# Kernel tuning notes

Hardware: AMD Instinct MI355X
Metric: run time of the kernel (lower is better)

Reference implementation:

```python
import jax, jax.numpy as jnp
import numpy as np

D_MODEL = 1024
NUM_HEADS = 16
DEPTH = D_MODEL // NUM_HEADS
MAX_LEN = 5000
B, S = 4, 1024


def _dense(x, W, b):
    return x @ W + b


def _split_heads(x, n_heads, depth):
    # [..., S, D] -> [..., H, S, depth]
    *lead, s, d = x.shape
    x = x.reshape(*lead, s, n_heads, depth)
    return jnp.swapaxes(x, -3, -2)


def setup_inputs() -> dict:
    key = jax.random.key(0)
    ks = jax.random.split(key, 12)
    w = 0.02  # glorot-ish scale to keep softmax logits sane
    inp = {
        'q': jax.random.normal(ks[0], (B, S, D_MODEL), jnp.float32),
        'k': jax.random.normal(ks[1], (B, S, D_MODEL), jnp.float32),
        'v': jax.random.normal(ks[2], (B, S, D_MODEL), jnp.float32),
        'Wq': jax.random.normal(ks[3], (D_MODEL, D_MODEL), jnp.float32) * w,
        'bq': jnp.zeros((D_MODEL,), jnp.float32),
        'Wk': jax.random.normal(ks[4], (D_MODEL, D_MODEL), jnp.float32) * w,
        'bk': jnp.zeros((D_MODEL,), jnp.float32),
        'Wv': jax.random.normal(ks[5], (D_MODEL, D_MODEL), jnp.float32) * w,
        'bv': jnp.zeros((D_MODEL,), jnp.float32),
        'Uq': jax.random.normal(ks[6], (D_MODEL, D_MODEL), jnp.float32) * w,
        'buq': jnp.zeros((D_MODEL,), jnp.float32),
        'Uk': jax.random.normal(ks[7], (D_MODEL, D_MODEL), jnp.float32) * w,
        'buk': jnp.zeros((D_MODEL,), jnp.float32),
        'pos_table': jax.random.normal(ks[8], (MAX_LEN, D_MODEL), jnp.float32) * w,
        'theta_cc': jnp.zeros((1, NUM_HEADS, 1, 1), jnp.float32),
        'theta_co': jnp.zeros((1, NUM_HEADS, 1, 1), jnp.float32),
        'theta_oc': jnp.zeros((1, NUM_HEADS, 1, 1), jnp.float32),
        'Wo': jax.random.normal(ks[9], (D_MODEL, D_MODEL), jnp.float32) * w,
        'bo': jnp.zeros((D_MODEL,), jnp.float32),
    }
    return inp


def reference(q, k, v, Wq, bq, Wk, bk, Wv, bv, Uq, buq, Uk, buk,
              pos_table, theta_cc, theta_co, theta_oc, Wo, bo):
    b, s, d = q.shape
    # content projections -> [B,H,S,depth]
    q_c = _split_heads(_dense(q, Wq, bq), NUM_HEADS, DEPTH)
    k_c = _split_heads(_dense(k, Wk, bk), NUM_HEADS, DEPTH)
    v_c = _split_heads(_dense(v, Wv, bv), NUM_HEADS, DEPTH)
    content_scores = jnp.einsum('bhqd,bhkd->bhqk', q_c, k_c)

    # untied positional scores (shared across batch): [1,H,S,S]
    pos_emb = pos_table[:s]                               # [S,D]
    q_p = _split_heads(_dense(pos_emb, Uq, buq)[None], NUM_HEADS, DEPTH)
    k_p = _split_heads(_dense(pos_emb, Uk, buk)[None], NUM_HEADS, DEPTH)
    pos_scores = jnp.einsum('bhqd,bhkd->bhqk', q_p, k_p)  # [1,H,S,S]

    # CLS-row/col overrides with learnable thetas
    pos_scores = pos_scores.at[:, :, 1:, 0:1].set(jnp.broadcast_to(theta_oc, (1, NUM_HEADS, s - 1, 1)))
    pos_scores = pos_scores.at[:, :, 0:1, 1:].set(jnp.broadcast_to(theta_co, (1, NUM_HEADS, 1, s - 1)))
    pos_scores = pos_scores.at[:, :, 0:1, 0:1].set(theta_cc)

    scores = (content_scores + pos_scores) / jnp.sqrt(jnp.float32(DEPTH))
    attn = jax.nn.softmax(scores, axis=-1)
    out = jnp.einsum('bhqk,bhkd->bhqd', attn, v_c)        # [B,H,S,depth]
    out = jnp.swapaxes(out, 1, 2).reshape(b, s, d)        # [B,S,D]
    return _dense(out, Wo, bo)
```

## Files before the change

kernel.cpp:

```cpp
#include <hip/hip_runtime.h>
#include <hip/hip_bf16.h>

typedef __hip_bfloat16 bf16;
typedef unsigned short u16;
typedef __attribute__((ext_vector_type(8))) short short8;
typedef __attribute__((ext_vector_type(4))) float f32x4;

#define D_MODEL 1024
#define NUM_HEADS 16
#define DEPTH 64
#define BATCH 4
#define SEQ 1024
#define BS (BATCH * SEQ)

__device__ __forceinline__ float ldDyn(const void* p, size_t i, int isbf) {
  return isbf ? __bfloat162float(((const bf16*)p)[i]) : ((const float*)p)[i];
}
__device__ __forceinline__ u16 f2bf(float f) {
  bf16 h = __float2bfloat16(f);
  return *(u16*)&h;
}
__device__ __forceinline__ void gl2lds16(const void* g, void* l) {
  __builtin_amdgcn_global_load_lds((const __attribute__((address_space(1))) unsigned int*)g,
                                   (__attribute__((address_space(3))) unsigned int*)l, 16, 0, 0);
}

__global__ void detect_kernel(const u16* __restrict__ q, int* __restrict__ flag) {
  if (threadIdx.x == 0 && blockIdx.x == 0) {
    int sane = 0;
    for (int i = 0; i < 64; ++i) {
      u16 h = q[2 * i];
      int e = (h >> 7) & 0xFF;
      if (e >= 100 && e <= 150) ++sane;
    }
    *flag = (sane >= 48) ? 1 : 0;
  }
}

__global__ __launch_bounds__(256) void convert_in(
    const void* __restrict__ q, const void* __restrict__ k, const void* __restrict__ v,
    const void* __restrict__ pos, u16* __restrict__ Qb, u16* __restrict__ Kb,
    u16* __restrict__ Vb, u16* __restrict__ Pb, const int* __restrict__ flagp) {
  const int isbf = *flagp;
  const int z = blockIdx.z;
  const void* src = (z == 0) ? q : (z == 1) ? k : (z == 2) ? v : pos;
  u16* dst = (z == 0) ? Qb : (z == 1) ? Kb : (z == 2) ? Vb : Pb;
  const size_t n8 = ((z == 3) ? (size_t)SEQ * D_MODEL : (size_t)BS * D_MODEL) / 8;
  for (size_t i = (size_t)blockIdx.x * 256 + threadIdx.x; i < n8; i += (size_t)gridDim.x * 256) {
    short8 o;
    if (isbf) {
      o = ((const short8*)src)[i];
    } else {
      const float4* f = (const float4*)src + 2 * i;
      float4 lo = f[0], hi = f[1];
      u16* pv = (u16*)&o;
      pv[0] = f2bf(lo.x); pv[1] = f2bf(lo.y); pv[2] = f2bf(lo.z); pv[3] = f2bf(lo.w);
      pv[4] = f2bf(hi.x); pv[5] = f2bf(hi.y); pv[6] = f2bf(hi.z); pv[7] = f2bf(hi.w);
    }
    ((short8*)dst)[i] = o;
  }
}

__global__ __launch_bounds__(256) void transpose_w(
    const void* W0, const void* W1, const void* W2, const void* W3, const void* W4,
    const void* W5, u16* __restrict__ WT, const int* __restrict__ flagp) {
  const int isbf = *flagp;
  const int z = blockIdx.z;
  const void* W = (z == 0) ? W0 : (z == 1) ? W1 : (z == 2) ? W2
                 : (z == 3) ? W3 : (z == 4) ? W4 : W5;
  u16* out = WT + (size_t)z * D_MODEL * D_MODEL;
  __shared__ u16 tile[32][33];
  const int t = threadIdx.x;
  const int tx = t & 31, ty = t >> 5;
  const int r0 = blockIdx.y * 32, c0 = blockIdx.x * 32;
#pragma unroll
  for (int i = 0; i < 4; ++i) {
    size_t gi = (size_t)(r0 + ty + 8 * i) * D_MODEL + c0 + tx;
    tile[ty + 8 * i][tx] = isbf ? ((const u16*)W)[gi] : f2bf(((const float*)W)[gi]);
  }
  __syncthreads();
#pragma unroll
  for (int i = 0; i < 4; ++i)
    out[(size_t)(c0 + ty + 8 * i) * D_MODEL + r0 + tx] = tile[tx][ty + 8 * i];
}

struct GArgs {
  const u16* A[5];
  const u16* W[5];
  const void* bias[5];
  void* C[5];
  int Mr[5];
  int om[5];
};

__global__ __launch_bounds__(256, 3) void gemm_mfma(GArgs ga, const int* __restrict__ flagp) {
  const int isbf = *flagp;
  const int z = blockIdx.z;
  const int M = ga.Mr[z];
  const int lin = blockIdx.x + 8 * blockIdx.y;
  const int xcd = lin & 7;
  const int loc = lin >> 3;
  const int rowb = (loc & 3) * 8 + xcd;
  const int colb = loc >> 2;
  const int row0 = rowb * 128, col0 = colb * 128;
  if (row0 >= M) return;
  const u16* A = ga.A[z];
  const u16* WT = ga.W[z];
  const void* bias = ga.bias[z];
  void* C = ga.C[z];
  const int omode = ga.om[z];

  __shared__ short As[3][128][32];
  __shared__ short Bs[3][128][32];
  const int t = threadIdx.x;
  const int wave = t >> 6, lane = t & 63;
  const int quad = lane >> 4, c16 = lane & 15;
  const int wrow = wave >> 1, wcol = wave & 1;

  f32x4 acc[4][4];
#pragma unroll
  for (int mt = 0; mt < 4; ++mt)
#pragma unroll
    for (int nt = 0; nt < 4; ++nt) acc[mt][nt] = {0.f, 0.f, 0.f, 0.f};

#define G_STAGE(K0, BUF)                                                                  \
  {                                                                                       \
    _Pragma("unroll") for (int i = 0; i < 2; ++i) {                                       \
      int L = t + 256 * i;                                                                \
      int r = L >> 2;                                                                     \
      int kc = (L & 3) ^ ((r + (r >> 2)) & 3);                                            \
      gl2lds16(WT + (size_t)(col0 + r) * 1024 + (K0) + kc * 8,                            \
               (char*)&Bs[BUF][0][0] + (size_t)(i * 256 + wave * 64) * 16);               \
      gl2lds16(A + (size_t)(row0 + r) * 1024 + (K0) + kc * 8,                             \
               (char*)&As[BUF][0][0] + (size_t)(i * 256 + wave * 64) * 16);               \
    }                                                                                     \
  }

  const int fsw = (c16 + (c16 >> 2)) & 3;

#define COMPUTE(BUF)                                                                      \
  {                                                                                       \
    short8 af[4], bfv[4];                                                                 \
    _Pragma("unroll") for (int mt = 0; mt < 4; ++mt)                                      \
        af[mt] = *(const short8*)&As[BUF][wrow * 64 + mt * 16 + c16][((quad ^ fsw) * 8)]; \
    _Pragma("unroll") for (int nt = 0; nt < 4; ++nt)                                      \
        bfv[nt] = *(const short8*)&Bs[BUF][wcol * 64 + nt * 16 + c16][((quad ^ fsw) * 8)];\
    _Pragma("unroll") for (int nt = 0; nt < 4; ++nt)                                      \
      _Pragma("unroll") for (int mt = 0; mt < 4; ++mt)                                    \
          acc[mt][nt] =                                                                   \
              __builtin_amdgcn_mfma_f32_16x16x32_bf16(af[mt], bfv[nt], acc[mt][nt], 0, 0, 0); \
  }

  G_STAGE(0, 0);
  G_STAGE(32, 1);
#pragma unroll
  for (int kk = 0; kk < 31; ++kk) {
    asm volatile("s_waitcnt vmcnt(4)\n\ts_barrier" ::: "memory");
    if (kk < 30) G_STAGE((kk + 2) * 32, (kk + 2) % 3);
    COMPUTE(kk % 3);
  }
  asm volatile("s_waitcnt vmcnt(0)\n\ts_barrier" ::: "memory");
  COMPUTE(1);
#undef G_STAGE
#undef COMPUTE

#pragma unroll
  for (int nt = 0; nt < 4; ++nt) {
    int gc = col0 + wcol * 64 + nt * 16 + c16;
    float bb = ldDyn(bias, gc, isbf);
#pragma unroll
    for (int mt = 0; mt < 4; ++mt) {
      int gr0 = row0 + wrow * 64 + mt * 16 + quad * 4;
      if (omode == 2) {
        __attribute__((ext_vector_type(4))) short pk;
#pragma unroll
        for (int r = 0; r < 4; ++r) pk[r] = (short)f2bf(acc[mt][nt][r] + bb);
        *(__attribute__((ext_vector_type(4))) short*)&((u16*)C)[(size_t)gc * M + gr0] = pk;
      } else if (omode == 1 || isbf) {
#pragma unroll
        for (int r = 0; r < 4; ++r)
          ((bf16*)C)[(size_t)(gr0 + r) * 1024 + gc] = __float2bfloat16(acc[mt][nt][r] + bb);
      } else {
#pragma unroll
        for (int r = 0; r < 4; ++r)
          ((float*)C)[(size_t)(gr0 + r) * 1024 + gc] = acc[mt][nt][r] + bb;
      }
    }
  }
}

__global__ __launch_bounds__(256) void flash_attn(
    const bf16* __restrict__ Qc, const bf16* __restrict__ Kc, const bf16* __restrict__ VcT,
    const bf16* __restrict__ Qp, const bf16* __restrict__ Kp,
    const void* __restrict__ th_cc, const void* __restrict__ th_co,
    const void* __restrict__ th_oc, bf16* __restrict__ O, const int* __restrict__ flagp) {
  const int isbf = *flagp;
  const int h = blockIdx.x, b = blockIdx.y, qt = blockIdx.z;
  const int t = threadIdx.x, wave = t >> 6, lane = t & 63;
  const int quad = lane >> 4, c16 = lane & 15;

  __shared__ short Kt[2][64][128];
  __shared__ short Vt[2][64][64];
  __shared__ short Pt[4][16][64];

  const float tcc = ldDyn(th_cc, h, isbf);
  const float tco = ldDyn(th_co, h, isbf);
  const float toc = ldDyn(th_oc, h, isbf);

  const bf16* kcb = Kc + (size_t)b * SEQ * 1024 + h * 64;
  const bf16* kpb = Kp + h * 64;
  const bf16* vtb = VcT + (size_t)(h * 64) * BS + (size_t)b * SEQ;

  const int rwK = lane >> 4, kcK = lane & 15;
  const int rwV = lane >> 3, kcV = lane & 7;

#define STAGE_K(KT2, BUF)                                                              \
  {                                                                                    \
    _Pragma("unroll") for (int i = 0; i < 4; ++i) {                                    \
      int r = wave * 16 + i * 4 + rwK;                                                 \
      int c = kcK ^ (r & 15);                                                          \
      int key = (KT2)*64 + r;                                                          \
      const bf16* src = (c < 8) ? kcb + (size_t)key * 1024 + c * 8                     \
                                : kpb + (size_t)key * 1024 + c * 8 - 64;               \
      gl2lds16(src, &Kt[BUF][wave * 16 + i * 4][0]);                                   \
    }                                                                                  \
  }
#define STAGE_V(KT2, BUF)                                                              \
  {                                                                                    \
    _Pragma("unroll") for (int j = 0; j < 2; ++j) {                                    \
      int d = wave * 16 + j * 8 + rwV;                                                 \
      int c = kcV ^ (d & 7);                                                           \
      gl2lds16(vtb + (size_t)d * BS + (KT2)*64 + c * 8, &Vt[BUF][wave * 16 + j * 8][0]); \
    }                                                                                  \
  }

  short8 qf[2][4];
#pragma unroll
  for (int mt = 0; mt < 2; ++mt) {
    int qrow = qt * 128 + wave * 32 + mt * 16 + c16;
#pragma unroll
    for (int ks = 0; ks < 4; ++ks) {
      int d = ks * 32 + quad * 8;
      const bf16* src = (d < 64) ? Qc + ((size_t)(b * SEQ + qrow)) * 1024 + h * 64 + d
                                 : Qp + (size_t)qrow * 1024 + h * 64 + (d - 64);
      qf[mt][ks] = *(const short8*)src;
    }
    if (qrow == 0) {
      qf[mt][2] = (short8)0;
      qf[mt][3] = (short8)0;
    }
  }

  f32x4 accO[2][4];
#pragma unroll
  for (int mt = 0; mt < 2; ++mt)
#pragma unroll
    for (int nt = 0; nt < 4; ++nt) accO[mt][nt] = {0.f, 0.f, 0.f, 0.f};
  float lrow[2][4] = {{0.f, 0.f, 0.f, 0.f}, {0.f, 0.f, 0.f, 0.f}};

  STAGE_K(0, 0);
  STAGE_V(0, 0);
  __syncthreads();
  if (t < 8) *(short8*)&Kt[0][0][64 + t * 8] = (short8)0;
  __syncthreads();

  for (int kt = 0; kt < 16; ++kt) {
    const int cur = kt & 1, nxt = cur ^ 1;
    if (kt < 15) {
      STAGE_K(kt + 1, nxt);
      STAGE_V(kt + 1, nxt);
    }

    f32x4 accS[2][4];
#pragma unroll
    for (int mt = 0; mt < 2; ++mt)
#pragma unroll
      for (int nt = 0; nt < 4; ++nt) accS[mt][nt] = {0.f, 0.f, 0.f, 0.f};
    __builtin_amdgcn_s_setprio(1);
#pragma unroll
    for (int nt = 0; nt < 4; ++nt)
#pragma unroll
      for (int ks = 0; ks < 4; ++ks) {
        short8 kf = *(const short8*)&Kt[cur][nt * 16 + c16][((ks * 4 + quad) ^ c16) * 8];
#pragma unroll
        for (int mt = 0; mt < 2; ++mt)
          accS[mt][nt] = __builtin_amdgcn_mfma_f32_16x16x32_bf16(qf[mt][ks], kf, accS[mt][nt], 0, 0, 0);
      }
    __builtin_amdgcn_s_setprio(0);

    short8 vbreg[2][4];
#pragma unroll
    for (int ks2 = 0; ks2 < 2; ++ks2)
#pragma unroll
      for (int nt = 0; nt < 4; ++nt)
        vbreg[ks2][nt] =
            *(const short8*)&Vt[cur][nt * 16 + c16][(((ks2 * 4 + quad) ^ (c16 & 7)) & 7) * 8];

#pragma unroll
    for (int mt = 0; mt < 2; ++mt) {
      float s[4][4];
#pragma unroll
      for (int nt = 0; nt < 4; ++nt)
#pragma unroll
        for (int r = 0; r < 4; ++r) s[nt][r] = accS[mt][nt][r] * 0.125f;

      if (kt == 0 || (qt == 0 && wave == 0 && mt == 0)) {
#pragma unroll
        for (int nt = 0; nt < 4; ++nt)
#pragma unroll
          for (int r = 0; r < 4; ++r) {
            int kcol = kt * 64 + nt * 16 + c16;
            int qrow = qt * 128 + wave * 32 + mt * 16 + quad * 4 + r;
            float add = 0.f;
            if (qrow == 0 && kcol == 0) add = tcc;
            else if (qrow == 0) add = tco;
            else if (kcol == 0) add = toc;
            s[nt][r] += add * 0.125f;
          }
      }
#pragma unroll
      for (int nt = 0; nt < 4; ++nt)
#pragma unroll
        for (int r = 0; r < 4; ++r) {
          float p = __expf(s[nt][r]);
          lrow[mt][r] += p;
          int row = quad * 4 + r;
          int ch = nt * 2 + (c16 >> 3);
          Pt[wave][row][((ch ^ (row & 7)) * 8) + (c16 & 7)] = (short)f2bf(p);
        }
      __builtin_amdgcn_s_setprio(1);
#pragma unroll
      for (int ks2 = 0; ks2 < 2; ++ks2) {
        short8 pf = *(const short8*)&Pt[wave][c16][(((ks2 * 4 + quad) ^ (c16 & 7)) & 7) * 8];
#pragma unroll
        for (int nt = 0; nt < 4; ++nt)
          accO[mt][nt] = __builtin_amdgcn_mfma_f32_16x16x32_bf16(pf, vbreg[ks2][nt], accO[mt][nt], 0, 0, 0);
      }
      __builtin_amdgcn_s_setprio(0);
    }
    __syncthreads();
  }

#pragma unroll
  for (int d = 1; d < 16; d <<= 1)
#pragma unroll
    for (int mt = 0; mt < 2; ++mt)
#pragma unroll
      for (int r = 0; r < 4; ++r) lrow[mt][r] += __shfl_xor(lrow[mt][r], d, 64);

#pragma unroll
  for (int mt = 0; mt < 2; ++mt)
#pragma unroll
    for (int nt = 0; nt < 4; ++nt)
#pragma unroll
      for (int r = 0; r < 4; ++r) {
        int qrow = qt * 128 + wave * 32 + mt * 16 + quad * 4 + r;
        O[((size_t)(b * SEQ + qrow)) * 1024 + h * 64 + nt * 16 + c16] =
            __float2bfloat16(accO[mt][nt][r] / lrow[mt][r]);
      }
#undef STAGE_K
#undef STAGE_V
}

extern "C" void kernel_launch(void* const* d_in, const int* in_sizes, int n_in,
                              void* d_out, int out_size, void* d_ws, size_t ws_size,
                              hipStream_t stream) {
  const void* q = d_in[0];
  const void* k = d_in[1];
  const void* v = d_in[2];
  const void* Wq = d_in[3];
  const void* bq = d_in[4];
  const void* Wk = d_in[5];
  const void* bk = d_in[6];
  const void* Wv = d_in[7];
  const void* bv = d_in[8];
  const void* Uq = d_in[9];
  const void* buq = d_in[10];
  const void* Uk = d_in[11];
  const void* buk = d_in[12];
  const void* pos = d_in[13];
  const void* th_cc = d_in[14];
  const void* th_co = d_in[15];
  const void* th_oc = d_in[16];
  const void* Wo = d_in[17];
  const void* bo = d_in[18];

  const int M = BS;
  const size_t DD = (size_t)D_MODEL * D_MODEL;
  char* wsb = (char*)d_ws;
  int* flag = (int*)wsb;
  bf16* Qc = (bf16*)(wsb + 256);
  bf16* Kc = Qc + (size_t)M * D_MODEL;
  bf16* VcT = Kc + (size_t)M * D_MODEL;
  bf16* Qp = VcT + (size_t)M * D_MODEL;
  bf16* Kp = Qp + (size_t)SEQ * D_MODEL;
  u16* WT = (u16*)(Kp + (size_t)SEQ * D_MODEL);
  bf16* AO = (bf16*)WT;
  u16* Qb = WT + 6 * DD;
  u16* Kb = Qb + (size_t)M * D_MODEL;
  u16* Vb = Kb + (size_t)M * D_MODEL;
  u16* Pb = Vb + (size_t)M * D_MODEL;

  detect_kernel<<<1, 64, 0, stream>>>((const u16*)q, flag);

  dim3 blk(256);
  convert_in<<<dim3(512, 1, 4), blk, 0, stream>>>(q, k, v, pos, Qb, Kb, Vb, Pb, flag);
  transpose_w<<<dim3(32, 32, 6), blk, 0, stream>>>(Wq, Wk, Wv, Uq, Uk, Wo, WT, flag);

  GArgs g1 = {{Qb, Kb, Vb, Pb, Pb},
              {WT + 0 * DD, WT + 1 * DD, WT + 2 * DD, WT + 3 * DD, WT + 4 * DD},
              {bq, bk, bv, buq, buk},
              {Qc, Kc, VcT, Qp, Kp},
              {M, M, M, SEQ, SEQ},
              {1, 1, 2, 1, 1}};
  gemm_mfma<<<dim3(8, 32, 5), blk, 0, stream>>>(g1, flag);

  flash_attn<<<dim3(NUM_HEADS, BATCH, SEQ / 128), blk, 0, stream>>>(
      Qc, Kc, VcT, Qp, Kp, th_cc, th_co, th_oc, AO, flag);

  GArgs g2 = {{(const u16*)AO, (const u16*)AO, (const u16*)AO, (const u16*)AO, (const u16*)AO},
              {WT + 5 * DD, WT + 5 * DD, WT + 5 * DD, WT + 5 * DD, WT + 5 * DD},
              {bo, bo, bo, bo, bo},
              {d_out, d_out, d_out, d_out, d_out},
              {M, M, M, M, M},
              {0, 0, 0, 0, 0}};
  gemm_mfma<<<dim3(8, 32, 1), blk, 0, stream>>>(g2, flag);
}
```

Before: 279.2 us.

## Enlarge GEMM tile to 256x128 and merge prep kernels into one launch

The GEMM block tile grows from 128x128 to 256x128, with 8x4 MFMA accumulators per wave, a larger A staging buffer, and the wait count and grid sized to match. This raises arithmetic intensity per loaded B tile and halves the number of blocks. Separately, format detection, input conversion and weight transposition are merged into a single prep kernel to remove two launches. In exchange the GEMM uses more registers and LDS (occupancy hint drops to 2), and fewer blocks may underfill the CUs, especially for the 1024-row positional GEMMs.

```diff
diff --git a/kernel.cpp b/kernel.cpp
--- a/kernel.cpp
+++ b/kernel.cpp
@@ -25,63 +25,63 @@
                                    (__attribute__((address_space(3))) unsigned int*)l, 16, 0, 0);
 }
 
-__global__ void detect_kernel(const u16* __restrict__ q, int* __restrict__ flag) {
-  if (threadIdx.x == 0 && blockIdx.x == 0) {
-    int sane = 0;
-    for (int i = 0; i < 64; ++i) {
-      u16 h = q[2 * i];
-      int e = (h >> 7) & 0xFF;
-      if (e >= 100 && e <= 150) ++sane;
-    }
-    *flag = (sane >= 48) ? 1 : 0;
-  }
-}
-
-__global__ __launch_bounds__(256) void convert_in(
+__device__ __forceinline__ int detect_isbf(const u16* q) {
+  int sane = 0;
+#pragma unroll
+  for (int i = 0; i < 64; ++i) {
+    int e = (q[2 * i] >> 7) & 0xFF;
+    sane += (e >= 100 && e <= 150) ? 1 : 0;
+  }
+  return (sane >= 48) ? 1 : 0;
+}
+
+__global__ __launch_bounds__(256) void prep(
     const void* __restrict__ q, const void* __restrict__ k, const void* __restrict__ v,
-    const void* __restrict__ pos, u16* __restrict__ Qb, u16* __restrict__ Kb,
-    u16* __restrict__ Vb, u16* __restrict__ Pb, const int* __restrict__ flagp) {
-  const int isbf = *flagp;
+    const void* __restrict__ pos, const void* __restrict__ W0, const void* __restrict__ W1,
+    const void* __restrict__ W2, const void* __restrict__ W3, const void* __restrict__ W4,
+    const void* __restrict__ W5, u16* __restrict__ Qb, u16* __restrict__ Kb,
+    u16* __restrict__ Vb, u16* __restrict__ Pb, u16* __restrict__ WT,
+    int* __restrict__ flag) {
+  const int isbf = detect_isbf((const u16*)q);
   const int z = blockIdx.z;
-  const void* src = (z == 0) ? q : (z == 1) ? k : (z == 2) ? v : pos;
-  u16* dst = (z == 0) ? Qb : (z == 1) ? Kb : (z == 2) ? Vb : Pb;
-  const size_t n8 = ((z == 3) ? (size_t)SEQ * D_MODEL : (size_t)BS * D_MODEL) / 8;
-  for (size_t i = (size_t)blockIdx.x * 256 + threadIdx.x; i < n8; i += (size_t)gridDim.x * 256) {
-    short8 o;
-    if (isbf) {
-      o = ((const short8*)src)[i];
-    } else {
-      const float4* f = (const float4*)src + 2 * i;
-      float4 lo = f[0], hi = f[1];
-      u16* pv = (u16*)&o;
-      pv[0] = f2bf(lo.x); pv[1] = f2bf(lo.y); pv[2] = f2bf(lo.z); pv[3] = f2bf(lo.w);
-      pv[4] = f2bf(hi.x); pv[5] = f2bf(hi.y); pv[6] = f2bf(hi.z); pv[7] = f2bf(hi.w);
-    }
-    ((short8*)dst)[i] = o;
-  }
-}
-
-__global__ __launch_bounds__(256) void transpose_w(
-    const void* W0, const void* W1, const void* W2, const void* W3, const void* W4,
-    const void* W5, u16* __restrict__ WT, const int* __restrict__ flagp) {
-  const int isbf = *flagp;
-  const int z = blockIdx.z;
-  const void* W = (z == 0) ? W0 : (z == 1) ? W1 : (z == 2) ? W2
-                 : (z == 3) ? W3 : (z == 4) ? W4 : W5;
-  u16* out = WT + (size_t)z * D_MODEL * D_MODEL;
-  __shared__ u16 tile[32][33];
   const int t = threadIdx.x;
-  const int tx = t & 31, ty = t >> 5;
-  const int r0 = blockIdx.y * 32, c0 = blockIdx.x * 32;
-#pragma unroll
-  for (int i = 0; i < 4; ++i) {
-    size_t gi = (size_t)(r0 + ty + 8 * i) * D_MODEL + c0 + tx;
-    tile[ty + 8 * i][tx] = isbf ? ((const u16*)W)[gi] : f2bf(((const float*)W)[gi]);
-  }
-  __syncthreads();
-#pragma unroll
-  for (int i = 0; i < 4; ++i)
-    out[(size_t)(c0 + ty + 8 * i) * D_MODEL + r0 + tx] = tile[tx][ty + 8 * i];
+  if (z == 0 && blockIdx.x == 0 && t == 0) *flag = isbf;
+
+  if (z < 4) {
+    const void* src = (z == 0) ? q : (z == 1) ? k : (z == 2) ? v : pos;
+    u16* dst = (z == 0) ? Qb : (z == 1) ? Kb : (z == 2) ? Vb : Pb;
+    const size_t n8 = ((z == 3) ? (size_t)SEQ * D_MODEL : (size_t)BS * D_MODEL) / 8;
+    for (size_t i = (size_t)blockIdx.x * 256 + t; i < n8; i += (size_t)gridDim.x * 256) {
+      short8 o;
+      if (isbf) {
+        o = ((const short8*)src)[i];
+      } else {
+        const float4* f = (const float4*)src + 2 * i;
+        float4 lo = f[0], hi = f[1];
+        u16* pv = (u16*)&o;
+        pv[0] = f2bf(lo.x); pv[1] = f2bf(lo.y); pv[2] = f2bf(lo.z); pv[3] = f2bf(lo.w);
+        pv[4] = f2bf(hi.x); pv[5] = f2bf(hi.y); pv[6] = f2bf(hi.z); pv[7] = f2bf(hi.w);
+      }
+      ((short8*)dst)[i] = o;
+    }
+  } else {
+    const int w = z - 4;
+    const void* W = (w == 0) ? W0 : (w == 1) ? W1 : (w == 2) ? W2
+                   : (w == 3) ? W3 : (w == 4) ? W4 : W5;
+    u16* out = WT + (size_t)w * D_MODEL * D_MODEL;
+    __shared__ u16 tile[32][33];
+    const int tx = t & 31, ty = t >> 5;
+    const int r0 = (blockIdx.x >> 5) * 32, c0 = (blockIdx.x & 31) * 32;
+#pragma unroll
+    for (int i = 0; i < 4; ++i) {
+      size_t gi = (size_t)(r0 + ty + 8 * i) * D_MODEL + c0 + tx;
+      tile[ty + 8 * i][tx] = isbf ? ((const u16*)W)[gi] : f2bf(((const float*)W)[gi]);
+    }
+    __syncthreads();
+#pragma unroll
+    for (int i = 0; i < 4; ++i)
+      out[(size_t)(c0 + ty + 8 * i) * D_MODEL + r0 + tx] = tile[tx][ty + 8 * i];
+  }
 }
 
 struct GArgs {
@@ -93,16 +93,16 @@
   int om[5];
 };
 
-__global__ __launch_bounds__(256, 3) void gemm_mfma(GArgs ga, const int* __restrict__ flagp) {
+__global__ __launch_bounds__(256, 2) void gemm_mfma(GArgs ga, const int* __restrict__ flagp) {
   const int isbf = *flagp;
   const int z = blockIdx.z;
   const int M = ga.Mr[z];
   const int lin = blockIdx.x + 8 * blockIdx.y;
   const int xcd = lin & 7;
   const int loc = lin >> 3;
-  const int rowb = (loc & 3) * 8 + xcd;
-  const int colb = loc >> 2;
-  const int row0 = rowb * 128, col0 = colb * 128;
+  const int rowb = (loc & 1) * 8 + xcd;
+  const int colb = loc >> 1;
+  const int row0 = rowb * 256, col0 = colb * 128;
   if (row0 >= M) return;
   const u16* A = ga.A[z];
   const u16* WT = ga.W[z];
@@ -110,29 +110,34 @@
   void* C = ga.C[z];
   const int omode = ga.om[z];
 
-  __shared__ short As[3][128][32];
+  __shared__ short As[3][256][32];
   __shared__ short Bs[3][128][32];
   const int t = threadIdx.x;
   const int wave = t >> 6, lane = t & 63;
   const int quad = lane >> 4, c16 = lane & 15;
   const int wrow = wave >> 1, wcol = wave & 1;
 
-  f32x4 acc[4][4];
-#pragma unroll
-  for (int mt = 0; mt < 4; ++mt)
+  f32x4 acc[8][4];
+#pragma unroll
+  for (int mt = 0; mt < 8; ++mt)
 #pragma unroll
     for (int nt = 0; nt < 4; ++nt) acc[mt][nt] = {0.f, 0.f, 0.f, 0.f};
 
 #define G_STAGE(K0, BUF)                                                                  \
   {                                                                                       \
+    _Pragma("unroll") for (int i = 0; i < 4; ++i) {                                       \
+      int L = t + 256 * i;                                                                \
+      int r = L >> 2;                                                                     \
+      int kc = (L & 3) ^ ((r + (r >> 2)) & 3);                                            \
+      gl2lds16(A + (size_t)(row0 + r) * 1024 + (K0) + kc * 8,                             \
+               (char*)&As[BUF][0][0] + (size_t)(i * 256 + wave * 64) * 16);               \
+    }                                                                                     \
     _Pragma("unroll") for (int i = 0; i < 2; ++i) {                                       \
       int L = t + 256 * i;                                                                \
       int r = L >> 2;                                                                     \
       int kc = (L & 3) ^ ((r + (r >> 2)) & 3);                                            \
       gl2lds16(WT + (size_t)(col0 + r) * 1024 + (K0) + kc * 8,                            \
                (char*)&Bs[BUF][0][0] + (size_t)(i * 256 + wave * 64) * 16);               \
-      gl2lds16(A + (size_t)(row0 + r) * 1024 + (K0) + kc * 8,                             \
-               (char*)&As[BUF][0][0] + (size_t)(i * 256 + wave * 64) * 16);               \
     }                                                                                     \
   }
 
@@ -140,13 +145,13 @@
 
 #define COMPUTE(BUF)                                                                      \
   {                                                                                       \
-    short8 af[4], bfv[4];                                                                 \
-    _Pragma("unroll") for (int mt = 0; mt < 4; ++mt)                                      \
-        af[mt] = *(const short8*)&As[BUF][wrow * 64 + mt * 16 + c16][((quad ^ fsw) * 8)]; \
+    short8 af[8], bfv[4];                                                                 \
+    _Pragma("unroll") for (int mt = 0; mt < 8; ++mt)                                      \
+        af[mt] = *(const short8*)&As[BUF][wrow * 128 + mt * 16 + c16][((quad ^ fsw) * 8)];\
     _Pragma("unroll") for (int nt = 0; nt < 4; ++nt)                                      \
         bfv[nt] = *(const short8*)&Bs[BUF][wcol * 64 + nt * 16 + c16][((quad ^ fsw) * 8)];\
     _Pragma("unroll") for (int nt = 0; nt < 4; ++nt)                                      \
-      _Pragma("unroll") for (int mt = 0; mt < 4; ++mt)                                    \
+      _Pragma("unroll") for (int mt = 0; mt < 8; ++mt)                                    \
           acc[mt][nt] =                                                                   \
               __builtin_amdgcn_mfma_f32_16x16x32_bf16(af[mt], bfv[nt], acc[mt][nt], 0, 0, 0); \
   }
@@ -155,7 +160,7 @@
   G_STAGE(32, 1);
 #pragma unroll
   for (int kk = 0; kk < 31; ++kk) {
-    asm volatile("s_waitcnt vmcnt(4)\n\ts_barrier" ::: "memory");
+    asm volatile("s_waitcnt vmcnt(6)\n\ts_barrier" ::: "memory");
     if (kk < 30) G_STAGE((kk + 2) * 32, (kk + 2) % 3);
     COMPUTE(kk % 3);
   }
@@ -169,8 +174,8 @@
     int gc = col0 + wcol * 64 + nt * 16 + c16;
     float bb = ldDyn(bias, gc, isbf);
 #pragma unroll
-    for (int mt = 0; mt < 4; ++mt) {
-      int gr0 = row0 + wrow * 64 + mt * 16 + quad * 4;
+    for (int mt = 0; mt < 8; ++mt) {
+      int gr0 = row0 + wrow * 128 + mt * 16 + quad * 4;
       if (omode == 2) {
         __attribute__((ext_vector_type(4))) short pk;
 #pragma unroll
@@ -401,11 +406,9 @@
   u16* Vb = Kb + (size_t)M * D_MODEL;
   u16* Pb = Vb + (size_t)M * D_MODEL;
 
-  detect_kernel<<<1, 64, 0, stream>>>((const u16*)q, flag);
-
   dim3 blk(256);
-  convert_in<<<dim3(512, 1, 4), blk, 0, stream>>>(q, k, v, pos, Qb, Kb, Vb, Pb, flag);
-  transpose_w<<<dim3(32, 32, 6), blk, 0, stream>>>(Wq, Wk, Wv, Uq, Uk, Wo, WT, flag);
+  prep<<<dim3(1024, 1, 10), blk, 0, stream>>>(q, k, v, pos, Wq, Wk, Wv, Uq, Uk, Wo,
+                                              Qb, Kb, Vb, Pb, WT, flag);
 
   GArgs g1 = {{Qb, Kb, Vb, Pb, Pb},
               {WT + 0 * DD, WT + 1 * DD, WT + 2 * DD, WT + 3 * DD, WT + 4 * DD},
@@ -413,7 +416,7 @@
               {Qc, Kc, VcT, Qp, Kp},
               {M, M, M, SEQ, SEQ},
               {1, 1, 2, 1, 1}};
-  gemm_mfma<<<dim3(8, 32, 5), blk, 0, stream>>>(g1, flag);
+  gemm_mfma<<<dim3(8, 16, 5), blk, 0, stream>>>(g1, flag);
 
   flash_attn<<<dim3(NUM_HEADS, BATCH, SEQ / 128), blk, 0, stream>>>(
       Qc, Kc, VcT, Qp, Kp, th_cc, th_co, th_oc, AO, flag);
@@ -424,5 +427,5 @@
               {d_out, d_out, d_out, d_out, d_out},
               {M, M, M, M, M},
               {0, 0, 0, 0, 0}};
-  gemm_mfma<<<dim3(8, 32, 1), blk, 0, stream>>>(g2, flag);
-}
+  gemm_mfma<<<dim3(8, 16, 1), blk, 0, stream>>>(g2, flag);
+}
```

Result: slower. 301.3 us (+8.0%).
